# Kernel tuning notes

Hardware: AMD Instinct MI355X
Metric: run time of the kernel (lower is better)

The kernel has to match this reference:

```python
import jax, jax.numpy as jnp
import numpy as np

TEMP = 0.07
K = 16  # n_hard_negatives
NEG = jnp.float32(-1e30)


def setup_inputs() -> dict:
    key = jax.random.key(0)
    k1, k2 = jax.random.split(key)
    B, D = 8192, 512
    emb = jax.random.normal(k1, (B, D), dtype=jnp.float32)
    emb = emb / jnp.linalg.norm(emb, axis=1, keepdims=True)  # module expects L2-normalized
    labels = jax.random.randint(k2, (B,), 0, 2048, dtype=jnp.int64)
    return {"embeddings": emb, "labels": labels}


def _masked_topk(sim, valid, k):
    # sim: [B,B] float, valid: [B,B] bool -> (top values [B,k], per-slot validity [B,k])
    masked = jnp.where(valid, sim, NEG)
    top = jax.lax.top_k(masked, k)[0]
    count = jnp.sum(valid, axis=1)
    kmask = jnp.arange(k)[None, :] < jnp.minimum(count, k)[:, None]
    return top, kmask


def reference(embeddings, labels):
    B = embeddings.shape[0]
    sim = embeddings @ embeddings.T                      # [B,B]
    same = labels[:, None] == labels[None, :]
    eye = jnp.eye(B, dtype=bool)
    pos_mask = same & ~eye                               # positives exclude self
    neg_mask = ~same                                     # diagonal is 'same', so self excluded

    pos_count = jnp.sum(pos_mask, axis=1)
    neg_count = jnp.sum(neg_mask, axis=1)
    row_valid = (pos_count > 0) & (neg_count > 0)

    # semi-hard: negatives with sim < min positive sim
    pos_min = jnp.min(jnp.where(pos_mask, sim, -NEG), axis=1)     # [B]
    semi = neg_mask & (sim < pos_min[:, None])
    has_semi = jnp.any(semi, axis=1)

    top_semi, m_semi = _masked_topk(sim, semi, K)
    top_all, m_all = _masked_topk(sim, neg_mask, K)
    top = jnp.where(has_semi[:, None], top_semi, top_all)         # [B,K]
    kmask = jnp.where(has_semi[:, None], m_semi, m_all)           # [B,K]

    pos_sim = jnp.sum(jnp.where(pos_mask, sim, 0.0), axis=1) / jnp.maximum(pos_count, 1) / TEMP

    # masked logsumexp over the (variable-length) top-k hard negatives
    scaled = jnp.where(kmask, top / TEMP, NEG)
    m = jnp.max(scaled, axis=1)
    sum_exp = jnp.sum(jnp.where(kmask, jnp.exp(scaled - m[:, None]), 0.0), axis=1)
    lse = m + jnp.log(jnp.maximum(sum_exp, 1e-30))

    loss_i = -pos_sim + lse
    n_valid = jnp.sum(row_valid)
    return jnp.sum(jnp.where(row_valid, loss_i, 0.0)) / jnp.maximum(n_valid, 1)
```

## Files before the change

### kernel.cpp

```cpp
#include <hip/hip_runtime.h>
#include <stdint.h>
#include <stddef.h>


#define TEMPV 0.07f
#define NEGV -1e30f

typedef short v8s __attribute__((ext_vector_type(8)));
typedef float v4f __attribute__((ext_vector_type(4)));

__device__ __forceinline__ short f2bf(float f) {
  unsigned u = __float_as_uint(f);
  unsigned r = (u + 0x7fffu + ((u >> 16) & 1u)) >> 16;
  return (short)r;
}
__device__ __forceinline__ float bf2f(short s) {
  return __uint_as_float(((unsigned)(unsigned short)s) << 16);
}

__device__ __forceinline__ void gload16(const void* g, void* l) {
  __builtin_amdgcn_global_load_lds((const __attribute__((address_space(1))) unsigned*)g,
                                   (__attribute__((address_space(3))) unsigned*)l, 16, 0, 0);
}

struct SNet { unsigned char a[64]; unsigned char b[64]; int n; };
constexpr SNet mknet16() {
  SNet t{}; t.n = 0;
  for (int p = 1; p < 16; p <<= 1)
    for (int k = p; k >= 1; k >>= 1)
      for (int j = k % p; j + k < 16; j += 2 * k)
        for (int i = 0; i < k; ++i) {
          int x = i + j, y = i + j + k;
          if (y < 16 && (x / (2 * p)) == (y / (2 * p))) {
            t.a[t.n] = (unsigned char)x; t.b[t.n] = (unsigned char)y; ++t.n;
          }
        }
  return t;
}
constexpr SNet NET16 = mknet16();
constexpr int NETN = NET16.n;

__device__ __forceinline__ void sort16d(float (&V)[16]) {
#pragma unroll
  for (int c = 0; c < NETN; ++c) {
    const int x = NET16.a[c], y = NET16.b[c];
    float hi = fmaxf(V[x], V[y]);
    float lo = fminf(V[x], V[y]);
    V[x] = hi; V[y] = lo;
  }
}

__device__ __forceinline__ void clean16d(float (&V)[16]) {
#pragma unroll
  for (int s = 8; s >= 1; s >>= 1) {
#pragma unroll
    for (int i = 0; i < 16; ++i) {
      if ((i & s) == 0) {
        float hi = fmaxf(V[i], V[i + s]);
        float lo = fminf(V[i], V[i + s]);
        V[i] = hi; V[i + s] = lo;
      }
    }
  }
}

__device__ __forceinline__ void mergeld(float (&R)[16], const float (&M)[16]) {
#pragma unroll
  for (int i = 0; i < 8; ++i) {
    float a = fmaxf(M[i], R[15 - i]);
    float b = fmaxf(M[15 - i], R[i]);
    R[i] = a; R[15 - i] = b;
  }
  clean16d(R);
}

__device__ __forceinline__ void xmerge16(float (&M)[16], int mask) {
#pragma unroll
  for (int i = 0; i < 8; ++i) {
    float pa = __shfl_xor(M[15 - i], mask);
    float pb = __shfl_xor(M[i], mask);
    M[i] = fmaxf(M[i], pa);
    M[15 - i] = fmaxf(M[15 - i], pb);
  }
  clean16d(M);
}

__device__ __forceinline__ void ins16(float (&L)[16], float v) {
#pragma unroll
  for (int k = 0; k < 15; ++k) {
    float lo = fminf(v, L[k + 1]);
    float hi = fmaxf(v, L[k + 1]);
    L[k] = lo;
    v = hi;
  }
  L[15] = v;
}

__global__ void kconv(const float* __restrict__ emb, short* __restrict__ emb16,
                      float* lsum, int* nval, int* fbcnt) {
  int i = (blockIdx.x * 256 + threadIdx.x) * 4;
  float4 v = *(const float4*)(emb + i);
  short4 s;
  s.x = f2bf(v.x); s.y = f2bf(v.y); s.z = f2bf(v.z); s.w = f2bf(v.w);
  *(short4*)(emb16 + i) = s;
  if (blockIdx.x == 0 && threadIdx.x == 0) { *lsum = 0.f; *nval = 0; *fbcnt = 0; }
}

__global__ __launch_bounds__(256) void kprefhs(const int* __restrict__ lab,
                                               int* __restrict__ hist,
                                               int* __restrict__ start,
                                               int* __restrict__ rows) {
  __shared__ int h[2048];
  __shared__ int part[256];
  int t = threadIdx.x;
#pragma unroll
  for (int k = 0; k < 8; ++k) h[t * 8 + k] = 0;
  __syncthreads();
  for (int i = t; i < 8192; i += 256) atomicAdd(&h[lab[i]], 1);
  __syncthreads();
  int v[8], loc[8], s = 0;
#pragma unroll
  for (int k = 0; k < 8; ++k) v[k] = h[t * 8 + k];
#pragma unroll
  for (int k = 0; k < 8; ++k) { loc[k] = s; s += v[k]; }
  part[t] = s;
  __syncthreads();
  for (int off = 1; off < 256; off <<= 1) {
    int x = (t >= off) ? part[t - off] : 0;
    __syncthreads();
    part[t] += x;
    __syncthreads();
  }
  int base = (t > 0) ? part[t - 1] : 0;
#pragma unroll
  for (int k = 0; k < 8; ++k) {
    hist[t * 8 + k] = v[k];
    start[t * 8 + k] = base + loc[k];
  }
  __syncthreads();
#pragma unroll
  for (int k = 0; k < 8; ++k) h[t * 8 + k] = base + loc[k];
  __syncthreads();
  for (int i = t; i < 8192; i += 256) {
    int p = atomicAdd(&h[lab[i]], 1);
    rows[p] = i;
  }
}

__global__ __launch_bounds__(256) void kpos2(const short* __restrict__ emb16,
                                             const int* __restrict__ lab,
                                             const int* __restrict__ hist,
                                             const int* __restrict__ start,
                                             const int* __restrict__ rows,
                                             float* __restrict__ pmin,
                                             float* __restrict__ pterm,
                                             int* __restrict__ valid) {
  int t = threadIdx.x;
  int wv = t >> 6, lane = t & 63;
  int i = blockIdx.x * 4 + wv;
  int li = lab[i];
  int s0 = start[li], c = hist[li];
  float ei[8];
  v8s e = *(const v8s*)(emb16 + (size_t)i * 512 + lane * 8);
#pragma unroll
  for (int k = 0; k < 8; ++k) ei[k] = bf2f(e[k]);
  float smin = 1e30f, ssum = 0.f;
  for (int k = 0; k < c; ++k) {
    int j = rows[s0 + k];
    if (j == i) continue;
    v8s f = *(const v8s*)(emb16 + (size_t)j * 512 + lane * 8);
    float s = 0.f;
#pragma unroll
    for (int q = 0; q < 8; ++q) s += ei[q] * bf2f(f[q]);
#pragma unroll
    for (int off = 32; off; off >>= 1) s += __shfl_xor(s, off);
    smin = fminf(smin, s);
    ssum += s;
  }
  if (lane == 0) {
    int pc = c - 1, nc = 8192 - c;
    pmin[i] = smin;
    pterm[i] = ssum / (float)(pc > 0 ? pc : 1) / TEMPV;
    valid[i] = (pc > 0 && nc > 0) ? 1 : 0;
  }
}

__global__ __launch_bounds__(256, 2) void kgemm(const short* __restrict__ emb16,
                                                const int* __restrict__ lab,
                                                const float* __restrict__ pminA,
                                                float* __restrict__ Lsemi) {
  __shared__ __align__(16) short Cg[2][128][64];

  int t = threadIdx.x;
  int bid = blockIdx.x;
  int rb = bid >> 3, cb = bid & 7;
  int rowbase = rb * 128;
  int colblock = cb * 1024;

  int wv = t >> 6, l = t & 63;
  int l15 = l & 15, l4 = l >> 4;

  int myrow[2]; int rlab[2]; float pm[2];
#pragma unroll
  for (int fi = 0; fi < 2; ++fi) {
    myrow[fi] = rowbase + wv * 32 + fi * 16 + l15;
    rlab[fi] = lab[myrow[fi]];
    pm[fi] = pminA[myrow[fi]];
  }

  float RS[2][16];
#pragma unroll
  for (int fi = 0; fi < 2; ++fi)
#pragma unroll
    for (int k = 0; k < 16; ++k) RS[fi][k] = NEGV;

  v4f acc[8][2];
#pragma unroll
  for (int mi = 0; mi < 8; ++mi)
#pragma unroll
    for (int fi = 0; fi < 2; ++fi) acc[mi][fi] = (v4f)0.f;

#pragma unroll
  for (int q = 0; q < 4; ++q) {
    int e = q * 256 + t;
    int col = e >> 3, ch = e & 7;
    gload16(emb16 + ((size_t)(colblock + col) * 512 + ((ch ^ (col & 7)) * 8)),
            &Cg[0][col][ch * 8]);
  }
  v8s breg[2][2][2];
#pragma unroll
  for (int h = 0; h < 2; ++h)
#pragma unroll
    for (int fi = 0; fi < 2; ++fi)
      breg[0][h][fi] = *(const v8s*)(emb16 + (size_t)myrow[fi] * 512 + h * 32 + l4 * 8);
  asm volatile("s_waitcnt vmcnt(4)" ::: "memory");
  __builtin_amdgcn_s_barrier();

  const int apos0 = (l4 ^ (l15 & 7)) * 8;

  for (int ct = 0; ct < 8; ++ct) {
#pragma unroll
    for (int kst = 0; kst < 8; ++kst) {
      const int cur = kst & 1;
      v8s a0[8], a1[8];
#pragma unroll
      for (int mi = 0; mi < 8; ++mi)
        a0[mi] = *(const v8s*)&Cg[cur][mi * 16 + l15][apos0];
#pragma unroll
      for (int mi = 0; mi < 8; ++mi)
        a1[mi] = *(const v8s*)&Cg[cur][mi * 16 + l15][apos0 ^ 32];
      if (!(ct == 7 && kst == 7)) {
        const int nct = (kst == 7) ? ct + 1 : ct;
        const int nk = ((kst + 1) & 7) * 64;
#pragma unroll
        for (int q = 0; q < 4; ++q) {
          int e = q * 256 + t;
          int col = e >> 3, ch = e & 7;
          gload16(emb16 + ((size_t)(colblock + nct * 128 + col) * 512 + nk +
                           ((ch ^ (col & 7)) * 8)),
                  &Cg[cur ^ 1][col][ch * 8]);
        }
      }
      {
        const int nk = ((kst + 1) & 7) * 64;
#pragma unroll
        for (int h = 0; h < 2; ++h)
#pragma unroll
          for (int fi = 0; fi < 2; ++fi)
            breg[cur ^ 1][h][fi] =
                *(const v8s*)(emb16 + (size_t)myrow[fi] * 512 + nk + h * 32 + l4 * 8);
      }
      __builtin_amdgcn_s_setprio(1);
#pragma unroll
      for (int mi = 0; mi < 8; ++mi)
#pragma unroll
        for (int fi = 0; fi < 2; ++fi)
          acc[mi][fi] = __builtin_amdgcn_mfma_f32_16x16x32_bf16(
              a0[mi], breg[cur][0][fi], acc[mi][fi], 0, 0, 0);
#pragma unroll
      for (int mi = 0; mi < 8; ++mi)
#pragma unroll
        for (int fi = 0; fi < 2; ++fi)
          acc[mi][fi] = __builtin_amdgcn_mfma_f32_16x16x32_bf16(
              a1[mi], breg[cur][1][fi], acc[mi][fi], 0, 0, 0);
      __builtin_amdgcn_s_setprio(0);
      if (kst == 7) {
        const int mycolbase = colblock + ct * 128;
#pragma unroll
        for (int c = 0; c < 2; ++c) {
          int lc[4][4];
#pragma unroll
          for (int mm = 0; mm < 4; ++mm) {
            int4 q = *(const int4*)&lab[mycolbase + (c * 4 + mm) * 16 + l4 * 4];
            lc[mm][0] = q.x; lc[mm][1] = q.y; lc[mm][2] = q.z; lc[mm][3] = q.w;
          }
#pragma unroll
          for (int fi = 0; fi < 2; ++fi) {
            float S[16];
#pragma unroll
            for (int j = 0; j < 16; ++j) {
              const int mi = c * 4 + (j >> 2), r = j & 3;
              float v = acc[mi][fi][r];
              bool keep = (lc[j >> 2][r] != rlab[fi]) && (v < pm[fi]);
              S[j] = keep ? v : NEGV;
            }
            sort16d(S);
            mergeld(RS[fi], S);
          }
        }
#pragma unroll
        for (int mi = 0; mi < 8; ++mi)
#pragma unroll
          for (int fi = 0; fi < 2; ++fi) acc[mi][fi] = (v4f)0.f;
      }
      asm volatile("s_waitcnt vmcnt(4)" ::: "memory");
      __builtin_amdgcn_s_barrier();
    }
  }

#pragma unroll
  for (int fi = 0; fi < 2; ++fi) {
    xmerge16(RS[fi], 16);
    xmerge16(RS[fi], 32);
    if (l4 == 0) {
      size_t o = ((size_t)cb * 8192 + myrow[fi]) * 16;
#pragma unroll
      for (int k = 0; k < 4; ++k)
        *(float4*)&Lsemi[o + k * 4] = make_float4(RS[fi][k * 4], RS[fi][k * 4 + 1],
                                                  RS[fi][k * 4 + 2], RS[fi][k * 4 + 3]);
    }
  }
}

__global__ __launch_bounds__(256) void kfin(const float* __restrict__ Lsemi,
                                            const float* __restrict__ pterm,
                                            const int* __restrict__ valid,
                                            float* lsum, int* nval,
                                            int* fbcnt, int* fbrows) {
  int i = blockIdx.x * 256 + threadIdx.x;
  float S[16], M[16];
#pragma unroll
  for (int k = 0; k < 16; ++k) S[k] = Lsemi[(size_t)i * 16 + k];
  for (int c = 1; c < 8; ++c) {
    size_t o = ((size_t)c * 8192 + i) * 16;
#pragma unroll
    for (int k = 0; k < 16; ++k) M[k] = Lsemi[o + k];
    mergeld(S, M);
  }
  int vd = valid[i];
  bool hs = S[0] > -1e29f;
  float li = 0.f;
  if (vd && !hs) {
    int idx = atomicAdd(fbcnt, 1);
    fbrows[idx] = i;
  } else if (vd) {
    float m = S[0] / TEMPV;
    float se = 0.f;
#pragma unroll
    for (int k = 0; k < 16; ++k)
      if (S[k] > -1e29f) se += expf(S[k] / TEMPV - m);
    li = m + logf(se) - pterm[i];
  }
#pragma unroll
  for (int off = 32; off; off >>= 1) {
    li += __shfl_xor(li, off);
    vd += __shfl_xor(vd, off);
  }
  __shared__ float rsd[4];
  __shared__ int rid[4];
  int wv = threadIdx.x >> 6;
  if ((threadIdx.x & 63) == 0) { rsd[wv] = li; rid[wv] = vd; }
  __syncthreads();
  if (threadIdx.x == 0) {
    atomicAdd(lsum, rsd[0] + rsd[1] + rsd[2] + rsd[3]);
    atomicAdd(nval, rid[0] + rid[1] + rid[2] + rid[3]);
  }
}

__global__ __launch_bounds__(256) void kfallA(const short* __restrict__ emb16,
                                              const int* __restrict__ lab,
                                              const int* __restrict__ fbcnt,
                                              const int* __restrict__ fbrows,
                                              float* __restrict__ fbpart) {
  int nfb = *fbcnt;
  if (nfb > 2048) nfb = 2048;
  int nunits = nfb * 32;
  __shared__ short remb[512];
  __shared__ float sims[256];
  int t = threadIdx.x;
  for (int u = blockIdx.x; u < nunits; u += gridDim.x) {
    int f = u >> 5, j = u & 31;
    int row = fbrows[f];
    int rl = lab[row];
    __syncthreads();
    if (t < 64) *(v8s*)&remb[t * 8] = *(const v8s*)(emb16 + (size_t)row * 512 + t * 8);
    __syncthreads();
    int c = j * 256 + t;
    float sz[8];
#pragma unroll
    for (int z = 0; z < 8; ++z) sz[z] = 0.f;
#pragma unroll 4
    for (int q = 0; q < 64; ++q) {
      v8s e = *(const v8s*)(emb16 + (size_t)c * 512 + q * 8);
      v8s r = *(const v8s*)&remb[q * 8];
#pragma unroll
      for (int z = 0; z < 8; ++z) sz[z] += bf2f(e[z]) * bf2f(r[z]);
    }
    float s = ((sz[0] + sz[1]) + (sz[2] + sz[3])) + ((sz[4] + sz[5]) + (sz[6] + sz[7]));
    sims[t] = (lab[c] != rl) ? s : NEGV;
    __syncthreads();
    if (t < 64) {
      float M[16];
#pragma unroll
      for (int k = 0; k < 16; ++k) M[k] = NEGV;
      M[0] = sims[t]; M[1] = sims[64 + t]; M[2] = sims[128 + t]; M[3] = sims[192 + t];
      sort16d(M);
      xmerge16(M, 1); xmerge16(M, 2); xmerge16(M, 4);
      xmerge16(M, 8); xmerge16(M, 16); xmerge16(M, 32);
      if (t == 0) {
#pragma unroll
        for (int k = 0; k < 16; ++k) fbpart[(size_t)(f * 32 + j) * 16 + k] = M[k];
      }
    }
  }
}

__global__ __launch_bounds__(256) void kfallB(const short* __restrict__ emb16,
                                              const int* __restrict__ lab,
                                              const int* __restrict__ fbcnt,
                                              const int* __restrict__ fbrows,
                                              const float* __restrict__ fbpart,
                                              const float* __restrict__ pterm,
                                              float* lsum) {
  int nfb = *fbcnt;
  int gid = blockIdx.x * 256 + threadIdx.x;
  for (int f = gid; f < nfb; f += gridDim.x * 256) {
    int row = fbrows[f];
    float R[16];
    if (f < 2048) {
#pragma unroll
      for (int k = 0; k < 16; ++k) R[k] = fbpart[(size_t)(f * 32) * 16 + k];
      for (int j = 1; j < 32; ++j) {
        float M[16];
#pragma unroll
        for (int k = 0; k < 16; ++k) M[k] = fbpart[(size_t)(f * 32 + j) * 16 + k];
        mergeld(R, M);
      }
    } else {
      int rl = lab[row];
      float L[16];
#pragma unroll
      for (int k = 0; k < 16; ++k) L[k] = NEGV;
      for (int c = 0; c < 8192; ++c) {
        if (lab[c] == rl) continue;
        float s = 0.f;
        for (int q = 0; q < 64; ++q) {
          v8s e = *(const v8s*)(emb16 + (size_t)c * 512 + q * 8);
          v8s r = *(const v8s*)(emb16 + (size_t)row * 512 + q * 8);
#pragma unroll
          for (int z = 0; z < 8; ++z) s += bf2f(e[z]) * bf2f(r[z]);
        }
        if (s > L[0]) ins16(L, s);
      }
#pragma unroll
      for (int k = 0; k < 16; ++k) R[k] = L[15 - k];
    }
    float m = R[0] / TEMPV;
    float se = 0.f;
#pragma unroll
    for (int k = 0; k < 16; ++k)
      if (R[k] > -1e29f) se += expf(R[k] / TEMPV - m);
    float lse = m + logf(se);
    atomicAdd(lsum, lse - pterm[row]);
  }
}

__global__ void kout(const float* lsum, const int* nval, float* out) {
  if (threadIdx.x == 0 && blockIdx.x == 0)
    out[0] = lsum[0] / (float)(nval[0] > 0 ? nval[0] : 1);
}

extern "C" void kernel_launch(void* const* d_in, const int* in_sizes, int n_in,
                              void* d_out, int out_size, void* d_ws, size_t ws_size,
                              hipStream_t stream) {
  const float* emb = (const float*)d_in[0];
  const int* lab = (const int*)d_in[1];
  float* out = (float*)d_out;

  char* wsb = (char*)d_ws;
  short* emb16 = (short*)wsb;
  int* hist = (int*)(wsb + 8388608);
  int* start = (int*)(wsb + 8396800);
  int* rows = (int*)(wsb + 8404992);
  float* pmin = (float*)(wsb + 8437760);
  float* pterm = (float*)(wsb + 8470528);
  int* valid = (int*)(wsb + 8503296);
  float* LsemiW = (float*)(wsb + 8536064);
  int* fbcnt = (int*)(wsb + 12730368);
  int* fbrows = (int*)(wsb + 12730432);
  float* fbpart = (float*)(wsb + 12763200);
  float* lsum = (float*)(wsb + 16957504);
  int* nval = (int*)(wsb + 16957508);

  kconv<<<4096, 256, 0, stream>>>(emb, emb16, lsum, nval, fbcnt);
  kprefhs<<<1, 256, 0, stream>>>(lab, hist, start, rows);
  kpos2<<<2048, 256, 0, stream>>>(emb16, lab, hist, start, rows, pmin, pterm, valid);
  kgemm<<<512, 256, 0, stream>>>(emb16, lab, pmin, LsemiW);
  kfin<<<32, 256, 0, stream>>>(LsemiW, pterm, valid, lsum, nval, fbcnt, fbrows);
  kfallA<<<256, 256, 0, stream>>>(emb16, lab, fbcnt, fbrows, fbpart);
  kfallB<<<32, 256, 0, stream>>>(emb16, lab, fbcnt, fbrows, fbpart, pterm, lsum);
  kout<<<1, 64, 0, stream>>>(lsum, nval, out);
}
```

Measured before the change: 188.5 us.

## Halve GEMM row tile and keep full-K row operand resident in registers

The fused similarity/top-k GEMM kernel now processes 64 rows per block instead of 128, with one 16-row fragment per wave, and launches twice as many blocks. Each lane preloads its row's entire 512-wide bf16 row operand into registers up front, so the per-k-step global loads of the row operand go away. The wait before each barrier now drains all outstanding loads. In exchange, each column tile staged in LDS is reused by half as many rows, doubling column-tile traffic, and MFMA work per barrier is halved, so sync overhead weighs more relative to compute.

```diff
diff --git a/kernel.cpp b/kernel.cpp
--- a/kernel.cpp
+++ b/kernel.cpp
@@ -194,31 +194,31 @@
   int t = threadIdx.x;
   int bid = blockIdx.x;
   int rb = bid >> 3, cb = bid & 7;
-  int rowbase = rb * 128;
+  int rowbase = rb * 64;
   int colblock = cb * 1024;
 
   int wv = t >> 6, l = t & 63;
   int l15 = l & 15, l4 = l >> 4;
 
-  int myrow[2]; int rlab[2]; float pm[2];
-#pragma unroll
-  for (int fi = 0; fi < 2; ++fi) {
-    myrow[fi] = rowbase + wv * 32 + fi * 16 + l15;
-    rlab[fi] = lab[myrow[fi]];
-    pm[fi] = pminA[myrow[fi]];
-  }
-
-  float RS[2][16];
-#pragma unroll
-  for (int fi = 0; fi < 2; ++fi)
-#pragma unroll
-    for (int k = 0; k < 16; ++k) RS[fi][k] = NEGV;
-
-  v4f acc[8][2];
-#pragma unroll
-  for (int mi = 0; mi < 8; ++mi)
-#pragma unroll
-    for (int fi = 0; fi < 2; ++fi) acc[mi][fi] = (v4f)0.f;
+  int myrow = rowbase + wv * 16 + l15;
+  int rlab = lab[myrow];
+  float pm = pminA[myrow];
+
+  v8s brow[8][2];
+#pragma unroll
+  for (int kst = 0; kst < 8; ++kst)
+#pragma unroll
+    for (int h = 0; h < 2; ++h)
+      brow[kst][h] =
+          *(const v8s*)(emb16 + (size_t)myrow * 512 + kst * 64 + h * 32 + l4 * 8);
+
+  float RS[16];
+#pragma unroll
+  for (int k = 0; k < 16; ++k) RS[k] = NEGV;
+
+  v4f acc[8];
+#pragma unroll
+  for (int mi = 0; mi < 8; ++mi) acc[mi] = (v4f)0.f;
 
 #pragma unroll
   for (int q = 0; q < 4; ++q) {
@@ -227,13 +227,7 @@
     gload16(emb16 + ((size_t)(colblock + col) * 512 + ((ch ^ (col & 7)) * 8)),
             &Cg[0][col][ch * 8]);
   }
-  v8s breg[2][2][2];
-#pragma unroll
-  for (int h = 0; h < 2; ++h)
-#pragma unroll
-    for (int fi = 0; fi < 2; ++fi)
-      breg[0][h][fi] = *(const v8s*)(emb16 + (size_t)myrow[fi] * 512 + h * 32 + l4 * 8);
-  asm volatile("s_waitcnt vmcnt(4)" ::: "memory");
+  asm volatile("s_waitcnt vmcnt(0)" ::: "memory");
   __builtin_amdgcn_s_barrier();
 
   const int apos0 = (l4 ^ (l15 & 7)) * 8;
@@ -261,28 +255,15 @@
                   &Cg[cur ^ 1][col][ch * 8]);
         }
       }
-      {
-        const int nk = ((kst + 1) & 7) * 64;
-#pragma unroll
-        for (int h = 0; h < 2; ++h)
-#pragma unroll
-          for (int fi = 0; fi < 2; ++fi)
-            breg[cur ^ 1][h][fi] =
-                *(const v8s*)(emb16 + (size_t)myrow[fi] * 512 + nk + h * 32 + l4 * 8);
-      }
       __builtin_amdgcn_s_setprio(1);
 #pragma unroll
       for (int mi = 0; mi < 8; ++mi)
-#pragma unroll
-        for (int fi = 0; fi < 2; ++fi)
-          acc[mi][fi] = __builtin_amdgcn_mfma_f32_16x16x32_bf16(
-              a0[mi], breg[cur][0][fi], acc[mi][fi], 0, 0, 0);
+        acc[mi] = __builtin_amdgcn_mfma_f32_16x16x32_bf16(a0[mi], brow[kst][0],
+                                                          acc[mi], 0, 0, 0);
 #pragma unroll
       for (int mi = 0; mi < 8; ++mi)
-#pragma unroll
-        for (int fi = 0; fi < 2; ++fi)
-          acc[mi][fi] = __builtin_amdgcn_mfma_f32_16x16x32_bf16(
-              a1[mi], breg[cur][1][fi], acc[mi][fi], 0, 0, 0);
+        acc[mi] = __builtin_amdgcn_mfma_f32_16x16x32_bf16(a1[mi], brow[kst][1],
+                                                          acc[mi], 0, 0, 0);
       __builtin_amdgcn_s_setprio(0);
       if (kst == 7) {
         const int mycolbase = colblock + ct * 128;
@@ -294,41 +275,33 @@
             int4 q = *(const int4*)&lab[mycolbase + (c * 4 + mm) * 16 + l4 * 4];
             lc[mm][0] = q.x; lc[mm][1] = q.y; lc[mm][2] = q.z; lc[mm][3] = q.w;
           }
-#pragma unroll
-          for (int fi = 0; fi < 2; ++fi) {
-            float S[16];
-#pragma unroll
-            for (int j = 0; j < 16; ++j) {
-              const int mi = c * 4 + (j >> 2), r = j & 3;
-              float v = acc[mi][fi][r];
-              bool keep = (lc[j >> 2][r] != rlab[fi]) && (v < pm[fi]);
-              S[j] = keep ? v : NEGV;
-            }
-            sort16d(S);
-            mergeld(RS[fi], S);
+          float S[16];
+#pragma unroll
+          for (int j = 0; j < 16; ++j) {
+            const int mi = c * 4 + (j >> 2), r = j & 3;
+            float v = acc[mi][r];
+            bool keep = (lc[j >> 2][r] != rlab) && (v < pm);
+            S[j] = keep ? v : NEGV;
           }
+          sort16d(S);
+          mergeld(RS, S);
         }
 #pragma unroll
-        for (int mi = 0; mi < 8; ++mi)
-#pragma unroll
-          for (int fi = 0; fi < 2; ++fi) acc[mi][fi] = (v4f)0.f;
-      }
-      asm volatile("s_waitcnt vmcnt(4)" ::: "memory");
+        for (int mi = 0; mi < 8; ++mi) acc[mi] = (v4f)0.f;
+      }
+      asm volatile("s_waitcnt vmcnt(0)" ::: "memory");
       __builtin_amdgcn_s_barrier();
     }
   }
 
-#pragma unroll
-  for (int fi = 0; fi < 2; ++fi) {
-    xmerge16(RS[fi], 16);
-    xmerge16(RS[fi], 32);
-    if (l4 == 0) {
-      size_t o = ((size_t)cb * 8192 + myrow[fi]) * 16;
-#pragma unroll
-      for (int k = 0; k < 4; ++k)
-        *(float4*)&Lsemi[o + k * 4] = make_float4(RS[fi][k * 4], RS[fi][k * 4 + 1],
-                                                  RS[fi][k * 4 + 2], RS[fi][k * 4 + 3]);
-    }
+  xmerge16(RS, 16);
+  xmerge16(RS, 32);
+  if (l4 == 0) {
+    size_t o = ((size_t)cb * 8192 + myrow) * 16;
+#pragma unroll
+    for (int k = 0; k < 4; ++k)
+      *(float4*)&Lsemi[o + k * 4] =
+          make_float4(RS[k * 4], RS[k * 4 + 1], RS[k * 4 + 2], RS[k * 4 + 3]);
   }
 }
 
@@ -505,7 +478,7 @@
   kconv<<<4096, 256, 0, stream>>>(emb, emb16, lsum, nval, fbcnt);
   kprefhs<<<1, 256, 0, stream>>>(lab, hist, start, rows);
   kpos2<<<2048, 256, 0, stream>>>(emb16, lab, hist, start, rows, pmin, pterm, valid);
-  kgemm<<<512, 256, 0, stream>>>(emb16, lab, pmin, LsemiW);
+  kgemm<<<1024, 256, 0, stream>>>(emb16, lab, pmin, LsemiW);
   kfin<<<32, 256, 0, stream>>>(LsemiW, pterm, valid, lsum, nval, fbcnt, fbrows);
   kfallA<<<256, 256, 0, stream>>>(emb16, lab, fbcnt, fbrows, fbpart);
   kfallB<<<32, 256, 0, stream>>>(emb16, lab, fbcnt, fbrows, fbpart, pterm, lsum);
```

After: 177.9 us. 5.7% less time.
